# Performance work log

Measured on AMD Instinct MI355X. Metric: run time of the kernel, lower is better.

## Reference

```python
import jax, jax.numpy as jnp
import numpy as np

N_NODES = 100000
N_EDGES = 3200000
IN_C, HID_C, OUT_C = 128, 128, 64
NUM_GRAPHS = 1024


def sage_conv(x, edge_index, W_l, b_l, W_r):
    # PyG SAGEConv (aggr='mean', root_weight=True):
    #   out = lin_l(mean_{j in N(i)} x_j) + lin_r(x_i)
    src, dst = edge_index[0], edge_index[1]
    msg = x[src]                                             # [E, C] gather
    summed = jax.ops.segment_sum(msg, dst, num_segments=x.shape[0])
    cnt = jax.ops.segment_sum(jnp.ones((msg.shape[0],), x.dtype), dst,
                              num_segments=x.shape[0])
    mean_nb = summed / jnp.maximum(cnt, 1.0)[:, None]        # [N, C]
    return mean_nb @ W_l + b_l + x @ W_r


def setup_inputs() -> dict:
    key = jax.random.key(0)
    ks = jax.random.split(key, 8)
    x = jax.random.normal(ks[0], (N_NODES, IN_C), dtype=jnp.float32)
    edge_index = jax.random.randint(ks[1], (2, N_EDGES), 0, N_NODES, dtype=jnp.int64)
    batch = jnp.sort(jax.random.randint(ks[2], (N_NODES,), 0, NUM_GRAPHS, dtype=jnp.int64))
    s1 = 1.0 / np.sqrt(IN_C)
    s2 = 1.0 / np.sqrt(HID_C)
    W1_l = jax.random.uniform(ks[3], (IN_C, HID_C), jnp.float32, -s1, s1)
    b1 = jax.random.uniform(ks[4], (HID_C,), jnp.float32, -s1, s1)
    W1_r = jax.random.uniform(ks[5], (IN_C, HID_C), jnp.float32, -s1, s1)
    W2_l = jax.random.uniform(ks[6], (HID_C, OUT_C), jnp.float32, -s2, s2)
    b2 = jnp.zeros((OUT_C,), jnp.float32)
    W2_r = jax.random.uniform(ks[7], (HID_C, OUT_C), jnp.float32, -s2, s2)
    return {"x": x, "W1_l": W1_l, "b1": b1, "W1_r": W1_r,
            "W2_l": W2_l, "b2": b2, "W2_r": W2_r,
            "edge_index": edge_index, "batch": batch}


def reference(x, W1_l, b1, W1_r, W2_l, b2, W2_r, edge_index, batch):
    h = sage_conv(x, edge_index, W1_l, b1, W1_r)
    h = jax.nn.relu(h)
    # dropout is identity in eval mode (training=False)
    h = sage_conv(h, edge_index, W2_l, b2, W2_r)
    # global_mean_pool: segment mean over graph ids
    summed = jax.ops.segment_sum(h, batch, num_segments=NUM_GRAPHS)
    cnt = jax.ops.segment_sum(jnp.ones((h.shape[0],), h.dtype), batch,
                              num_segments=NUM_GRAPHS)
    return summed / jnp.maximum(cnt, 1.0)[:, None]           # [NUM_GRAPHS, OUT_C]
```

## Files before the change

kernel.cpp:

```cpp
#include <hip/hip_runtime.h>


constexpr int NN = 100000;
constexpr int NE = 3200000;
constexpr int C1 = 128;
constexpr int C2 = 64;
constexpr int NG = 1024;

constexpr int NBK = (NN + 511) >> 9;
constexpr int CAP = 18176;
constexpr int NSH = 13;

typedef unsigned int u32;
typedef unsigned short u16;
typedef unsigned char u8;
typedef _Float16 f16;
typedef f16 f16x8 __attribute__((ext_vector_type(8)));
typedef float f32x4 __attribute__((ext_vector_type(4)));

__device__ __forceinline__ float h2f(u32 bits16) {
  f16 h; u16 b = (u16)bits16;
  __builtin_memcpy(&h, &b, 2);
  return (float)h;
}
__device__ __forceinline__ u16 f2h(float f) {
  f16 h = (f16)f; u16 b;
  __builtin_memcpy(&b, &h, 2);
  return b;
}
__device__ __forceinline__ u32 packh2(float a, float b) {
  return (u32)f2h(a) | ((u32)f2h(b) << 16);
}
__device__ __forceinline__ u32 packq4(float a, float b, float c, float d) {
  int q = 0;
  q = __builtin_amdgcn_cvt_pk_fp8_f32(a, b, q, false);
  q = __builtin_amdgcn_cvt_pk_fp8_f32(c, d, q, true);
  return (u32)q;
}
__device__ __forceinline__ void acc4(u32 g, float& a0, float& a1,
                                     float& a2, float& a3) {
  const auto p = __builtin_amdgcn_cvt_pk_f32_fp8((int)g, false);
  const auto q = __builtin_amdgcn_cvt_pk_f32_fp8((int)g, true);
  a0 += p[0]; a1 += p[1]; a2 += q[0]; a3 += q[1];
}
__device__ __forceinline__ uint4 q8toh8(uint2 g) {
  const auto p0 = __builtin_amdgcn_cvt_pk_f32_fp8((int)g.x, false);
  const auto p1 = __builtin_amdgcn_cvt_pk_f32_fp8((int)g.x, true);
  const auto p2 = __builtin_amdgcn_cvt_pk_f32_fp8((int)g.y, false);
  const auto p3 = __builtin_amdgcn_cvt_pk_f32_fp8((int)g.y, true);
  uint4 o;
  o.x = packh2(p0[0], p0[1]);
  o.y = packh2(p1[0], p1[1]);
  o.z = packh2(p2[0], p2[1]);
  o.w = packh2(p3[0], p3[1]);
  return o;
}

__global__ __launch_bounds__(256)
void sage_x2hw(const float* __restrict__ x, u16* __restrict__ xh,
               u32* __restrict__ xq,
               const float* __restrict__ W1l, const float* __restrict__ W1r,
               const float* __restrict__ W2l, const float* __restrict__ W2r,
               u16* __restrict__ wt1, u16* __restrict__ wt2,
               int* __restrict__ gcur) {
  const int id = blockIdx.x * 256 + threadIdx.x;
  constexpr int NX = NN * 32;
  if (id < NX) {
    const float4 v = ((const float4*)x)[id];
    uint2 o;
    o.x = packh2(v.x, v.y);
    o.y = packh2(v.z, v.w);
    ((uint2*)xh)[id] = o;
    xq[id] = packq4(v.x, v.y, v.z, v.w);
  } else if (id < NX + 128 * 256) {
    const int id2 = id - NX;
    const int n = id2 >> 8, k = id2 & 255;
    const float v = (k < 128) ? W1l[k * 128 + n] : W1r[(k - 128) * 128 + n];
    wt1[id2] = f2h(v);
  } else if (id < NX + 128 * 256 + 128 * 128) {
    const int id3 = id - NX - 128 * 256;
    const int n = id3 >> 7, k = id3 & 127;
    const float v = (n < 64) ? W2l[k * 64 + n] : W2r[k * 64 + (n - 64)];
    wt2[id3] = f2h(v);
  } else if (id < NX + 128 * 256 + 128 * 128 + NBK) {
    const int b = id - NX - 128 * 256 - 128 * 128;
    gcur[b] = b * CAP;
  }
}

__global__ __launch_bounds__(256)
void sage_part(const int* __restrict__ esrc, const int* __restrict__ edst,
               int* __restrict__ gcur, u32* __restrict__ gpart) {
  __shared__ int h[NBK], cur[NBK];
  for (int i = threadIdx.x; i < NBK; i += 256) h[i] = 0;
  __syncthreads();
  const int e0 = blockIdx.x * 4096 + threadIdx.x * 4;
  int4 dv[4], sv[4];
  bool val[4];
#pragma unroll
  for (int j = 0; j < 4; ++j) {
    const int e = e0 + j * 1024;
    val[j] = (e < NE);
    if (val[j]) {
      dv[j] = *(const int4*)(edst + e);
      sv[j] = *(const int4*)(esrc + e);
    }
  }
#pragma unroll
  for (int j = 0; j < 4; ++j) {
    if (val[j]) {
      atomicAdd(&h[dv[j].x >> 9], 1);
      atomicAdd(&h[dv[j].y >> 9], 1);
      atomicAdd(&h[dv[j].z >> 9], 1);
      atomicAdd(&h[dv[j].w >> 9], 1);
    }
  }
  __syncthreads();
  for (int i = threadIdx.x; i < NBK; i += 256)
    cur[i] = h[i] ? atomicAdd(&gcur[i], h[i]) : 0;
  __syncthreads();
#pragma unroll
  for (int j = 0; j < 4; ++j) {
    if (val[j]) {
      int bk, p;
      bk = dv[j].x >> 9; p = atomicAdd(&cur[bk], 1);
      if (p < (bk + 1) * CAP) gpart[p] = ((u32)sv[j].x << 9) | (u32)(dv[j].x & 511);
      bk = dv[j].y >> 9; p = atomicAdd(&cur[bk], 1);
      if (p < (bk + 1) * CAP) gpart[p] = ((u32)sv[j].y << 9) | (u32)(dv[j].y & 511);
      bk = dv[j].z >> 9; p = atomicAdd(&cur[bk], 1);
      if (p < (bk + 1) * CAP) gpart[p] = ((u32)sv[j].z << 9) | (u32)(dv[j].z & 511);
      bk = dv[j].w >> 9; p = atomicAdd(&cur[bk], 1);
      if (p < (bk + 1) * CAP) gpart[p] = ((u32)sv[j].w << 9) | (u32)(dv[j].w & 511);
    }
  }
}

__global__ __launch_bounds__(256)
void sage_pscan(const int* __restrict__ gcur, int* __restrict__ bbase) {
  __shared__ int s[256];
  const int t = threadIdx.x;
  int c = (t < NBK) ? (gcur[t] - t * CAP) : 0;
  c = (c > CAP) ? CAP : c;
  s[t] = c;
  __syncthreads();
  for (int d = 1; d < 256; d <<= 1) {
    const int a = (t >= d) ? s[t - d] : 0;
    __syncthreads();
    s[t] += a;
    __syncthreads();
  }
  if (t < NBK) bbase[t] = s[t] - c;
  if (t == 255) bbase[NBK] = s[255];
}

__global__ __launch_bounds__(512)
void sage_bbuild(const int* __restrict__ bbase, const u32* __restrict__ gpart,
                 int* __restrict__ offs, int* __restrict__ csr) {
  __shared__ int cnt2[512 * NSH];
  __shared__ int ssc[512];
  const int b = blockIdx.x, t = threadIdx.x;
  const int c0 = bbase[b], cnt = bbase[b + 1] - c0;
  const u32* gp = gpart + (size_t)b * CAP;
  for (int i = t; i < 512 * NSH; i += 512) cnt2[i] = 0;
  __syncthreads();
  for (int e = t; e < cnt; e += 512) {
    const u32 pk = gp[e];
    atomicAdd(&cnt2[(pk & 511) * NSH + (pk >> 22)], 1);
  }
  __syncthreads();
  int deg = 0;
#pragma unroll
  for (int s = 0; s < NSH; ++s) deg += cnt2[t * NSH + s];
  ssc[t] = deg;
  __syncthreads();
  for (int d = 1; d < 512; d <<= 1) {
    const int a = (t >= d) ? ssc[t - d] : 0;
    __syncthreads();
    ssc[t] += a;
    __syncthreads();
  }
  const int pre = ssc[t] - deg;
  const int node = b * 512 + t;
  if (node < NN) offs[node] = c0 + pre;
  if (b == 0 && t == 0) offs[NN] = bbase[NBK];
  int run = c0 + pre;
#pragma unroll
  for (int s = 0; s < NSH; ++s) {
    const int c = cnt2[t * NSH + s];
    cnt2[t * NSH + s] = run;
    run += c;
  }
  __syncthreads();
  for (int e = t; e < cnt; e += 512) {
    const u32 pk = gp[e];
    const int p = atomicAdd(&cnt2[(pk & 511) * NSH + (pk >> 22)], 1);
    csr[p] = (int)(pk >> 9);
  }
}

__global__ __launch_bounds__(256)
void sage_agg1q(const int* __restrict__ offs, const int* __restrict__ csr,
                const u32* __restrict__ xq, u32* __restrict__ agg1) {
  const int node = blockIdx.x * 4 + (threadIdx.x >> 6);
  const int lane = threadIdx.x & 63;
  if (node >= NN) return;
  const int beg = offs[node], end = offs[node + 1];
  const int hf = lane >> 5, l = lane & 31;
  const u32* xb = xq + l;
  float a0 = 0, a1 = 0, a2 = 0, a3 = 0;
  int e = beg + hf;
  for (; e + 14 < end; e += 16) {
    const int i0 = csr[e],      i1 = csr[e + 2],  i2 = csr[e + 4],
              i3 = csr[e + 6],  i4 = csr[e + 8],  i5 = csr[e + 10],
              i6 = csr[e + 12], i7 = csr[e + 14];
    const u32 g0 = xb[(size_t)i0 * 32], g1 = xb[(size_t)i1 * 32],
              g2 = xb[(size_t)i2 * 32], g3 = xb[(size_t)i3 * 32],
              g4 = xb[(size_t)i4 * 32], g5 = xb[(size_t)i5 * 32],
              g6 = xb[(size_t)i6 * 32], g7 = xb[(size_t)i7 * 32];
    acc4(g0, a0, a1, a2, a3); acc4(g1, a0, a1, a2, a3);
    acc4(g2, a0, a1, a2, a3); acc4(g3, a0, a1, a2, a3);
    acc4(g4, a0, a1, a2, a3); acc4(g5, a0, a1, a2, a3);
    acc4(g6, a0, a1, a2, a3); acc4(g7, a0, a1, a2, a3);
  }
  for (; e < end; e += 2)
    acc4(xb[(size_t)csr[e] * 32], a0, a1, a2, a3);
  a0 += __shfl_xor(a0, 32);
  a1 += __shfl_xor(a1, 32);
  a2 += __shfl_xor(a2, 32);
  a3 += __shfl_xor(a3, 32);
  if (hf == 0) {
    const float inv = 1.0f / fmaxf((float)(end - beg), 1.0f);
    agg1[(size_t)node * 32 + l] = packq4(a0 * inv, a1 * inv, a2 * inv, a3 * inv);
  }
}

__global__ __launch_bounds__(256)
void sage_agg2q(const int* __restrict__ offs, const int* __restrict__ csr,
                const u32* __restrict__ tq, u16* __restrict__ agg2h) {
  const int node = blockIdx.x * 4 + (threadIdx.x >> 6);
  const int lane = threadIdx.x & 63;
  if (node >= NN) return;
  const int beg = offs[node], end = offs[node + 1];
  const int grp = lane >> 4, l = lane & 15;
  const u32* tb = tq + l;
  float a0 = 0, a1 = 0, a2 = 0, a3 = 0;
  int e = beg + grp;
  for (; e + 28 < end; e += 32) {
    const int i0 = csr[e],      i1 = csr[e + 4],  i2 = csr[e + 8],
              i3 = csr[e + 12], i4 = csr[e + 16], i5 = csr[e + 20],
              i6 = csr[e + 24], i7 = csr[e + 28];
    const u32 g0 = tb[(size_t)i0 * 16], g1 = tb[(size_t)i1 * 16],
              g2 = tb[(size_t)i2 * 16], g3 = tb[(size_t)i3 * 16],
              g4 = tb[(size_t)i4 * 16], g5 = tb[(size_t)i5 * 16],
              g6 = tb[(size_t)i6 * 16], g7 = tb[(size_t)i7 * 16];
    acc4(g0, a0, a1, a2, a3); acc4(g1, a0, a1, a2, a3);
    acc4(g2, a0, a1, a2, a3); acc4(g3, a0, a1, a2, a3);
    acc4(g4, a0, a1, a2, a3); acc4(g5, a0, a1, a2, a3);
    acc4(g6, a0, a1, a2, a3); acc4(g7, a0, a1, a2, a3);
  }
  for (; e < end; e += 4)
    acc4(tb[(size_t)csr[e] * 16], a0, a1, a2, a3);
  a0 += __shfl_xor(a0, 16); a0 += __shfl_xor(a0, 32);
  a1 += __shfl_xor(a1, 16); a1 += __shfl_xor(a1, 32);
  a2 += __shfl_xor(a2, 16); a2 += __shfl_xor(a2, 32);
  a3 += __shfl_xor(a3, 16); a3 += __shfl_xor(a3, 32);
  if (lane < 16) {
    const float inv = 1.0f / fmaxf((float)(end - beg), 1.0f);
    uint2 o;
    o.x = packh2(a0 * inv, a1 * inv);
    o.y = packh2(a2 * inv, a3 * inv);
    *(uint2*)(agg2h + (size_t)node * 64 + l * 4) = o;
  }
}

__global__ __launch_bounds__(256)
void sage_mgemm12(const u32* __restrict__ A1q, const u16* __restrict__ A2,
                  const u16* __restrict__ wt1, const u16* __restrict__ wt2,
                  const float* __restrict__ bias,
                  u16* __restrict__ O, u8* __restrict__ tqb) {
  __shared__ __align__(16) u16 As[2][64][128];
  const int t = threadIdx.x;
  const int r0 = blockIdx.x * 64;
#pragma unroll
  for (int i = 0; i < 4; ++i) {
    const int id = i * 256 + t;
    const int row = id >> 4, c = id & 15;
    int gr = r0 + row; gr = (gr < NN) ? gr : NN - 1;
    const uint2 g = *(const uint2*)(A1q + (size_t)gr * 32 + c * 2);
    *(uint4*)(&As[0][row][(c ^ (row & 7)) * 8]) = q8toh8(g);
  }
#pragma unroll
  for (int i = 0; i < 4; ++i) {
    const int id = i * 256 + t;
    const int row = id >> 4, c = id & 15;
    int gr = r0 + row; gr = (gr < NN) ? gr : NN - 1;
    const uint4 v = *(const uint4*)(A2 + (size_t)gr * 128 + c * 8);
    *(uint4*)(&As[1][row][(c ^ (row & 7)) * 8]) = v;
  }
  __syncthreads();
  const int w = t >> 6, l = t & 63;
  const int lr = l & 15, lk = l >> 4;
  const int rowl = w * 16 + lr;
  f32x4 acc[8];
#pragma unroll
  for (int c = 0; c < 8; ++c) acc[c] = (f32x4){0.f, 0.f, 0.f, 0.f};
#pragma unroll
  for (int kt = 0; kt < 8; ++kt) {
    const int buf = kt >> 2, kk = kt & 3;
    const int ch = (kk * 4 + lk) ^ (rowl & 7);
    const f16x8 a = *(const f16x8*)(&As[buf][rowl][ch * 8]);
#pragma unroll
    for (int c = 0; c < 8; ++c) {
      const f16x8 b = *(const f16x8*)(wt1 + ((c * 16 + lr) * 256 + kt * 32 + lk * 8));
      acc[c] = __builtin_amdgcn_mfma_f32_16x16x32_f16(a, b, acc[c], 0, 0, 0);
    }
  }
  __syncthreads();
#pragma unroll
  for (int c = 0; c < 8; ++c) {
    const int col = c * 16 + lr;
    const float bv = bias[col];
    const int chb = col >> 3, within = col & 7;
#pragma unroll
    for (int j = 0; j < 4; ++j) {
      const int row = w * 16 + lk * 4 + j;
      As[0][row][((chb ^ (row & 7)) << 3) + within] =
          f2h(fmaxf(acc[c][j] + bv, 0.f));
    }
  }
  __syncthreads();
#pragma unroll
  for (int c = 0; c < 8; ++c) acc[c] = (f32x4){0.f, 0.f, 0.f, 0.f};
#pragma unroll
  for (int kt = 0; kt < 4; ++kt) {
    const int ch = (kt * 4 + lk) ^ (rowl & 7);
    const f16x8 a = *(const f16x8*)(&As[0][rowl][ch * 8]);
#pragma unroll
    for (int c = 0; c < 8; ++c) {
      const f16x8 b = *(const f16x8*)(wt2 + ((c * 16 + lr) * 128 + kt * 32 + lk * 8));
      acc[c] = __builtin_amdgcn_mfma_f32_16x16x32_f16(a, b, acc[c], 0, 0, 0);
    }
  }
#pragma unroll
  for (int c = 0; c < 8; ++c) {
    const int col = c * 16 + lr;
#pragma unroll
    for (int j = 0; j < 4; ++j) {
      const int row = r0 + w * 16 + lk * 4 + j;
      if (row < NN) {
        if (col < 64) {
          const int pk = __builtin_amdgcn_cvt_pk_fp8_f32(acc[c][j], acc[c][j], 0, false);
          tqb[(size_t)row * 64 + col] = (u8)pk;
        } else {
          O[(size_t)row * 128 + col] = f2h(acc[c][j]);
        }
      }
    }
  }
}

__global__ __launch_bounds__(256)
void sage_pool2(const u16* __restrict__ o128, const u16* __restrict__ agg2h,
                const float* __restrict__ b2, const int* __restrict__ batch,
                float* __restrict__ pool, int* __restrict__ gcnt) {
  const int t = threadIdx.x;
  const int c = t & 63, sl = t >> 6;
  const int n0 = blockIdx.x * 128;
  const float bv = b2[c];
  float acc = 0.f;
  int curg = -1, cnt = 0;
  for (int n = n0 + sl; n < n0 + 128 && n < NN; n += 4) {
    const int g = batch[n];
    const float v = h2f(o128[(size_t)n * 128 + 64 + c]) +
                    h2f(agg2h[(size_t)n * 64 + c]) + bv;
    if (g != curg) {
      if (curg >= 0) {
        atomicAdd(&pool[curg * C2 + c], acc);
        if (c == 0) atomicAdd(&gcnt[curg], cnt);
      }
      curg = g; acc = v; cnt = 1;
    } else {
      acc += v; cnt += 1;
    }
  }
  if (curg >= 0) {
    atomicAdd(&pool[curg * C2 + c], acc);
    if (c == 0) atomicAdd(&gcnt[curg], cnt);
  }
}

__global__ __launch_bounds__(256)
void sage_out(const float* __restrict__ pool, const int* __restrict__ gcnt,
              float* __restrict__ out) {
  const int i = blockIdx.x * 256 + threadIdx.x;
  if (i >= NG * C2) return;
  out[i] = pool[i] / fmaxf((float)gcnt[i >> 6], 1.0f);
}

extern "C" void kernel_launch(void* const* d_in, const int* in_sizes, int n_in,
                              void* d_out, int out_size, void* d_ws, size_t ws_size,
                              hipStream_t stream) {
  (void)in_sizes; (void)n_in; (void)out_size; (void)ws_size;
  const float* x     = (const float*)d_in[0];
  const float* W1l   = (const float*)d_in[1];
  const float* b1    = (const float*)d_in[2];
  const float* W1r   = (const float*)d_in[3];
  const float* W2l   = (const float*)d_in[4];
  const float* b2    = (const float*)d_in[5];
  const float* W2r   = (const float*)d_in[6];
  const int*   ei    = (const int*)d_in[7];
  const int*   batch = (const int*)d_in[8];
  const int* esrc = ei;
  const int* edst = ei + NE;
  float* out = (float*)d_out;

  char* base = (char*)d_ws;
  size_t off = 0;
  auto take = [&](size_t bytes) -> char* {
    char* p = base + off;
    off += (bytes + 255) & ~(size_t)255;
    return p;
  };
  int* bbase    = (int*)take((size_t)(NBK + 1) * 4);
  int* gcur     = (int*)take((size_t)NBK * 4);
  int* offs     = (int*)take((size_t)(NN + 1) * 4);
  int* csr      = (int*)take((size_t)NE * 4);
  char* bufA    = take((size_t)NN * 256);
  char* bufB    = take((size_t)NN * 256);
  char* bufC    = take((size_t)NBK * CAP * 4 + (size_t)NN * 128);
  float* pool   = (float*)take((size_t)NG * C2 * 4);
  int*  gcnt    = (int*)take((size_t)NG * 4);
  u16*  wt1     = (u16*)take((size_t)128 * 256 * 2);
  u16*  wt2     = (u16*)take((size_t)128 * 128 * 2);

  u16*   xh    = (u16*)bufA;
  u16*   o128  = (u16*)bufA;
  u32*   agg1  = (u32*)bufB;
  u16*   agg2h = (u16*)bufB;
  u8*    tqb   = (u8*)(bufB + (size_t)NN * 128);
  u32*   gpart = (u32*)bufC;
  u32*   xq    = (u32*)(bufC + (size_t)NBK * CAP * 4);

  const size_t zbytes = (size_t)((char*)gcnt + (size_t)NG * 4 - (char*)pool);
  hipMemsetAsync(pool, 0, zbytes, stream);

  sage_x2hw<<<(NN * 32 + 128 * 256 + 128 * 128 + NBK + 255) / 256, 256, 0,
              stream>>>(x, xh, xq, W1l, W1r, W2l, W2r, wt1, wt2, gcur);

  const int PB = (NE + 4095) / 4096;
  sage_part<<<PB, 256, 0, stream>>>(esrc, edst, gcur, gpart);
  sage_pscan<<<1, 256, 0, stream>>>(gcur, bbase);
  sage_bbuild<<<NBK, 512, 0, stream>>>(bbase, gpart, offs, csr);

  sage_agg1q<<<(NN + 3) / 4, 256, 0, stream>>>(offs, csr, xq, agg1);

  sage_mgemm12<<<(NN + 63) / 64, 256, 0, stream>>>(agg1, xh, wt1, wt2, b1,
                                                   o128, tqb);

  sage_agg2q<<<(NN + 3) / 4, 256, 0, stream>>>(offs, csr, (const u32*)tqb, agg2h);

  sage_pool2<<<(NN + 127) / 128, 256, 0, stream>>>(o128, agg2h, b2, batch, pool, gcnt);
  sage_out<<<(NG * C2 + 255) / 256, 256, 0, stream>>>(pool, gcnt, out);
}
```

Before: 334.1 us.

## Split fused MLP GEMM tiles by output columns and keep weights in registers

The fused two-layer MFMA kernel now has each wave own a 32-column slice of the output across all 64 rows, instead of 16 rows across all 128 columns. Each wave loads its weight fragments for both GEMMs into registers once, with the first layer's loads issued before the A-tile staging. This removes the repeated global and L2 weight reads inside the MFMA loop. In exchange, each A fragment is now read from LDS by every wave, and the register-held weights raise register pressure, which may lower occupancy.

```diff
diff --git a/kernel.cpp b/kernel.cpp
--- a/kernel.cpp
+++ b/kernel.cpp
@@ -281,6 +281,16 @@
   __shared__ __align__(16) u16 As[2][64][128];
   const int t = threadIdx.x;
   const int r0 = blockIdx.x * 64;
+  const int w = t >> 6, l = t & 63;
+  const int lr = l & 15, lk = l >> 4;
+
+  f16x8 B1[2][8];
+#pragma unroll
+  for (int j = 0; j < 2; ++j)
+#pragma unroll
+    for (int kt = 0; kt < 8; ++kt)
+      B1[j][kt] = *(const f16x8*)(wt1 + (((2 * w + j) * 16 + lr) * 256 + kt * 32 + lk * 8));
+
 #pragma unroll
   for (int i = 0; i < 4; ++i) {
     const int id = i * 256 + t;
@@ -298,64 +308,81 @@
     *(uint4*)(&As[1][row][(c ^ (row & 7)) * 8]) = v;
   }
   __syncthreads();
-  const int w = t >> 6, l = t & 63;
-  const int lr = l & 15, lk = l >> 4;
-  const int rowl = w * 16 + lr;
-  f32x4 acc[8];
-#pragma unroll
-  for (int c = 0; c < 8; ++c) acc[c] = (f32x4){0.f, 0.f, 0.f, 0.f};
-#pragma unroll
-  for (int kt = 0; kt < 8; ++kt) {
-    const int buf = kt >> 2, kk = kt & 3;
-    const int ch = (kk * 4 + lk) ^ (rowl & 7);
-    const f16x8 a = *(const f16x8*)(&As[buf][rowl][ch * 8]);
-#pragma unroll
-    for (int c = 0; c < 8; ++c) {
-      const f16x8 b = *(const f16x8*)(wt1 + ((c * 16 + lr) * 256 + kt * 32 + lk * 8));
-      acc[c] = __builtin_amdgcn_mfma_f32_16x16x32_f16(a, b, acc[c], 0, 0, 0);
-    }
-  }
-  __syncthreads();
-#pragma unroll
-  for (int c = 0; c < 8; ++c) {
-    const int col = c * 16 + lr;
+
+  f32x4 acc[4][2];
+#pragma unroll
+  for (int rt = 0; rt < 4; ++rt)
+#pragma unroll
+    for (int j = 0; j < 2; ++j) acc[rt][j] = (f32x4){0.f, 0.f, 0.f, 0.f};
+#pragma unroll
+  for (int rt = 0; rt < 4; ++rt) {
+    const int ra = rt * 16 + lr;
+#pragma unroll
+    for (int kt = 0; kt < 8; ++kt) {
+      const int buf = kt >> 2, kk = kt & 3;
+      const f16x8 a = *(const f16x8*)(&As[buf][ra][((kk * 4 + lk) ^ (ra & 7)) * 8]);
+      acc[rt][0] = __builtin_amdgcn_mfma_f32_16x16x32_f16(a, B1[0][kt], acc[rt][0], 0, 0, 0);
+      acc[rt][1] = __builtin_amdgcn_mfma_f32_16x16x32_f16(a, B1[1][kt], acc[rt][1], 0, 0, 0);
+    }
+  }
+
+  f16x8 B2[2][4];
+#pragma unroll
+  for (int j = 0; j < 2; ++j)
+#pragma unroll
+    for (int kt = 0; kt < 4; ++kt)
+      B2[j][kt] = *(const f16x8*)(wt2 + (((2 * w + j) * 16 + lr) * 128 + kt * 32 + lk * 8));
+
+  __syncthreads();
+
+#pragma unroll
+  for (int j = 0; j < 2; ++j) {
+    const int col = (2 * w + j) * 16 + lr;
     const float bv = bias[col];
     const int chb = col >> 3, within = col & 7;
 #pragma unroll
-    for (int j = 0; j < 4; ++j) {
-      const int row = w * 16 + lk * 4 + j;
-      As[0][row][((chb ^ (row & 7)) << 3) + within] =
-          f2h(fmaxf(acc[c][j] + bv, 0.f));
-    }
-  }
-  __syncthreads();
-#pragma unroll
-  for (int c = 0; c < 8; ++c) acc[c] = (f32x4){0.f, 0.f, 0.f, 0.f};
-#pragma unroll
-  for (int kt = 0; kt < 4; ++kt) {
-    const int ch = (kt * 4 + lk) ^ (rowl & 7);
-    const f16x8 a = *(const f16x8*)(&As[0][rowl][ch * 8]);
-#pragma unroll
-    for (int c = 0; c < 8; ++c) {
-      const f16x8 b = *(const f16x8*)(wt2 + ((c * 16 + lr) * 128 + kt * 32 + lk * 8));
-      acc[c] = __builtin_amdgcn_mfma_f32_16x16x32_f16(a, b, acc[c], 0, 0, 0);
-    }
-  }
-#pragma unroll
-  for (int c = 0; c < 8; ++c) {
-    const int col = c * 16 + lr;
-#pragma unroll
-    for (int j = 0; j < 4; ++j) {
-      const int row = r0 + w * 16 + lk * 4 + j;
-      if (row < NN) {
-        if (col < 64) {
-          const int pk = __builtin_amdgcn_cvt_pk_fp8_f32(acc[c][j], acc[c][j], 0, false);
-          tqb[(size_t)row * 64 + col] = (u8)pk;
-        } else {
-          O[(size_t)row * 128 + col] = f2h(acc[c][j]);
+    for (int rt = 0; rt < 4; ++rt)
+#pragma unroll
+      for (int r = 0; r < 4; ++r) {
+        const int row = rt * 16 + lk * 4 + r;
+        As[0][row][((chb ^ (row & 7)) << 3) + within] =
+            f2h(fmaxf(acc[rt][j][r] + bv, 0.f));
+      }
+  }
+  __syncthreads();
+
+  f32x4 acc2[4][2];
+#pragma unroll
+  for (int rt = 0; rt < 4; ++rt)
+#pragma unroll
+    for (int j = 0; j < 2; ++j) acc2[rt][j] = (f32x4){0.f, 0.f, 0.f, 0.f};
+#pragma unroll
+  for (int rt = 0; rt < 4; ++rt) {
+    const int ra = rt * 16 + lr;
+#pragma unroll
+    for (int kt = 0; kt < 4; ++kt) {
+      const f16x8 a = *(const f16x8*)(&As[0][ra][((kt * 4 + lk) ^ (ra & 7)) * 8]);
+      acc2[rt][0] = __builtin_amdgcn_mfma_f32_16x16x32_f16(a, B2[0][kt], acc2[rt][0], 0, 0, 0);
+      acc2[rt][1] = __builtin_amdgcn_mfma_f32_16x16x32_f16(a, B2[1][kt], acc2[rt][1], 0, 0, 0);
+    }
+  }
+#pragma unroll
+  for (int j = 0; j < 2; ++j) {
+    const int col = (2 * w + j) * 16 + lr;
+#pragma unroll
+    for (int rt = 0; rt < 4; ++rt)
+#pragma unroll
+      for (int r = 0; r < 4; ++r) {
+        const int row = r0 + rt * 16 + lk * 4 + r;
+        if (row < NN) {
+          if (col < 64) {
+            const int pk = __builtin_amdgcn_cvt_pk_fp8_f32(acc2[rt][j][r], acc2[rt][j][r], 0, false);
+            tqb[(size_t)row * 64 + col] = (u8)pk;
+          } else {
+            O[(size_t)row * 128 + col] = f2h(acc2[rt][j][r]);
+          }
         }
       }
-    }
   }
 }
 
```

New measurement: 281.3 us. -15.8%, faster.
